# Kernel tuning notes

Measured on AMD Instinct MI355X. Metric: run time of the kernel, lower is better.

## Reference

```python
import jax, jax.numpy as jnp
import numpy as np

NUM_HEADS = 16
R_MIN = 16
R_MAX = 64


def setup_inputs() -> dict:
    key = jax.random.key(0)
    ks = jax.random.split(key, 12)
    bs, S, H = 4, 2048, 1024
    hidden_states = jax.random.normal(ks[0], (bs, S, H), dtype=jnp.float32)
    # Linear layers: y = x @ W.T + b (torch convention, W is [out, in])
    wscale = 1.0 / np.sqrt(H)
    Wq = jax.random.normal(ks[1], (H, H), dtype=jnp.float32) * wscale
    bq = jnp.zeros((H,), dtype=jnp.float32)
    Wk = jax.random.normal(ks[2], (H, H), dtype=jnp.float32) * wscale
    bk = jnp.zeros((H,), dtype=jnp.float32)
    Wv = jax.random.normal(ks[3], (H, H), dtype=jnp.float32) * wscale
    bv = jnp.zeros((H,), dtype=jnp.float32)
    Wo = jax.random.normal(ks[4], (H, H), dtype=jnp.float32) * wscale
    bo = jnp.zeros((H,), dtype=jnp.float32)
    # xavier_uniform for proj_k/proj_v over last two dims (seq_len, r_max)
    xs = float(np.sqrt(6.0 / (S + R_MAX)))
    proj_k = jax.random.uniform(ks[5], (NUM_HEADS, S, R_MAX), dtype=jnp.float32, minval=-xs, maxval=xs)
    proj_v = jax.random.uniform(ks[6], (NUM_HEADS, S, R_MAX), dtype=jnp.float32, minval=-xs, maxval=xs)
    return {
        'hidden_states': hidden_states,
        'Wq': Wq, 'bq': bq, 'Wk': Wk, 'bk': bk, 'Wv': Wv, 'bv': bv,
        'Wo': Wo, 'bo': bo, 'proj_k': proj_k, 'proj_v': proj_v,
    }


def reference(hidden_states, Wq, bq, Wk, bk, Wv, bv, Wo, bo, proj_k, proj_v):
    bs, S, H = hidden_states.shape
    nh = NUM_HEADS
    hd = H // nh

    def heads(x):  # [b,s,H] -> [b,h,s,d]
        return x.reshape(bs, S, nh, hd).transpose(0, 2, 1, 3)

    q = heads(hidden_states @ Wq.T + bq)
    k = heads(hidden_states @ Wk.T + bk)
    v = heads(hidden_states @ Wv.T + bv)

    # dynamic rank from per-sample variance (torch .var is unbiased -> ddof=1)
    batch_var = jnp.var(hidden_states.reshape(bs, -1), axis=1, ddof=1)
    var_norm = (batch_var - batch_var.min()) / (batch_var.max() - batch_var.min() + 1e-6)
    curr_r = jnp.round(R_MIN + var_norm.mean() * (R_MAX - R_MIN)).astype(jnp.int32)

    # low-rank projection of K/V along sequence; compute full r_max, mask at softmax
    key_proj = jnp.einsum('bhld,hlk->bhkd', k, proj_k)      # [b,h,R,d]
    value_proj = jnp.einsum('bhld,hlk->bhkd', v, proj_v)    # [b,h,R,d]

    scores = jnp.einsum('bhsd,bhkd->bhsk', q, key_proj) / jnp.sqrt(jnp.float32(hd))
    rank_mask = jnp.arange(R_MAX) < curr_r                  # [R]
    scores = jnp.where(rank_mask, scores, -jnp.inf)
    attn_probs = jax.nn.softmax(scores, axis=-1)            # zeros beyond curr_r
    # dropout is identity in eval mode
    context = jnp.einsum('bhsk,bhkd->bhsd', attn_probs, value_proj)
    context = context.transpose(0, 2, 1, 3).reshape(bs, S, H)
    output = context @ Wo.T + bo
    return output, attn_probs, curr_r
```

## Files before the change

kernel.cpp:

```cpp
#include <hip/hip_runtime.h>


typedef unsigned short u16;
typedef short s16x8 __attribute__((ext_vector_type(8)));
typedef unsigned short u16x8 __attribute__((ext_vector_type(8)));
typedef unsigned short u16x4 __attribute__((ext_vector_type(4)));
typedef float f32x4 __attribute__((ext_vector_type(4)));

#define GLL16(gp, lp) __builtin_amdgcn_global_load_lds( \
    (const __attribute__((address_space(1))) void*)(gp), \
    (__attribute__((address_space(3))) void*)(lp), 16, 0, 0)

__device__ __forceinline__ u16 f2bf(float f) {
    unsigned u = __float_as_uint(f);
    u += 0x7fffu + ((u >> 16) & 1u);
    return (u16)(u >> 16);
}

__device__ __forceinline__ f32x4 mfma16(s16x8 a, s16x8 b, f32x4 c) {
    return __builtin_amdgcn_mfma_f32_16x16x32_bf16(a, b, c, 0, 0, 0);
}

__global__ __launch_bounds__(256) void prep_k(const float* __restrict__ hs,
        u16* __restrict__ hsb, double* __restrict__ red,
        const float* __restrict__ w0, const float* __restrict__ w1,
        const float* __restrict__ w2, const float* __restrict__ w3,
        u16* __restrict__ wout,
        const float* __restrict__ p0, const float* __restrict__ p1,
        u16* __restrict__ q0, u16* __restrict__ q1,
        const float* __restrict__ bq, const float* __restrict__ bk,
        const float* __restrict__ bv, float* __restrict__ biascat) {
    __shared__ float tl[64][65];
    __shared__ double sa[256], sb[256];
    int bid = blockIdx.x, t = threadIdx.x;
    if (bid < 1024) {
        size_t base = (size_t)bid * 8192;
        double s = 0.0, s2 = 0.0;
        #pragma unroll
        for (int i = 0; i < 4; ++i) {
            size_t idx = base + (size_t)i * 2048 + (size_t)t * 8;
            float4 a = *(const float4*)(hs + idx);
            float4 c = *(const float4*)(hs + idx + 4);
            s  += (double)a.x + (double)a.y + (double)a.z + (double)a.w
                + (double)c.x + (double)c.y + (double)c.z + (double)c.w;
            s2 += (double)a.x * a.x + (double)a.y * a.y + (double)a.z * a.z + (double)a.w * a.w
                + (double)c.x * c.x + (double)c.y * c.y + (double)c.z * c.z + (double)c.w * c.w;
            u16x8 o;
            o[0] = f2bf(a.x); o[1] = f2bf(a.y); o[2] = f2bf(a.z); o[3] = f2bf(a.w);
            o[4] = f2bf(c.x); o[5] = f2bf(c.y); o[6] = f2bf(c.z); o[7] = f2bf(c.w);
            *(u16x8*)(hsb + idx) = o;
        }
        sa[t] = s; sb[t] = s2;
        __syncthreads();
        for (int o = 128; o > 0; o >>= 1) {
            if (t < o) { sa[t] += sa[t + o]; sb[t] += sb[t + o]; }
            __syncthreads();
        }
        if (t == 0) { red[bid * 2] = sa[0]; red[bid * 2 + 1] = sb[0]; }
    } else if (bid < 3072) {
        int bid2 = bid - 1024;
        int mat = bid2 >> 9;
        int off = ((bid2 & 511) * 256 + t) * 8;
        const float* src = (mat == 0) ? w0 : (mat == 1) ? w1 : (mat == 2) ? w2 : w3;
        float4 a = *(const float4*)(src + off);
        float4 c = *(const float4*)(src + off + 4);
        u16x8 o;
        o[0] = f2bf(a.x); o[1] = f2bf(a.y); o[2] = f2bf(a.z); o[3] = f2bf(a.w);
        o[4] = f2bf(c.x); o[5] = f2bf(c.y); o[6] = f2bf(c.z); o[7] = f2bf(c.w);
        *(u16x8*)(wout + (size_t)mat * 1048576 + off) = o;
    } else if (bid < 4096) {
        int bid2 = bid - 3072;
        int which = bid2 >> 9, bi = bid2 & 511;
        const float* p = which ? p1 : p0;
        u16* pt = which ? q1 : q0;
        int h = bi >> 5, lb = bi & 31;
        {
            int l = t >> 2, r0 = (t & 3) * 16;
            const float* src = p + ((size_t)(h * 2048 + lb * 64 + l)) * 64 + r0;
            #pragma unroll
            for (int u = 0; u < 4; ++u) {
                float4 v = *(const float4*)(src + u * 4);
                tl[l][r0 + u * 4 + 0] = v.x; tl[l][r0 + u * 4 + 1] = v.y;
                tl[l][r0 + u * 4 + 2] = v.z; tl[l][r0 + u * 4 + 3] = v.w;
            }
        }
        __syncthreads();
        {
            int r = t >> 2, l0 = (t & 3) * 16;
            u16x8 o0, o1;
            #pragma unroll
            for (int j = 0; j < 8; ++j) { o0[j] = f2bf(tl[l0 + j][r]); o1[j] = f2bf(tl[l0 + 8 + j][r]); }
            u16* dst = pt + ((size_t)(h * 64 + r)) * 2048 + lb * 64 + l0;
            *(u16x8*)dst = o0;
            *(u16x8*)(dst + 8) = o1;
        }
    } else {
        for (int i = t; i < 3072; i += 256) {
            float v = (i < 1024) ? bq[i] : (i < 2048) ? bk[i - 1024] : bv[i - 2048];
            biascat[i] = v;
        }
    }
}

__global__ __launch_bounds__(512, 2) void qkv_gemm_k(const u16* __restrict__ Ag,
        const u16* __restrict__ Wcat, const float* __restrict__ biascat,
        u16* __restrict__ C) {
    __shared__ u16 lds[61440];
    int bid = blockIdx.x;
    int swz = (bid & 7) * 32 + (bid >> 3);
    int bm = swz >> 3, bn = swz & 7;
    int t = threadIdx.x, lane = t & 63, w = t >> 6, wr = w >> 2, wc = w & 3;

    int srow = w * 16 + (lane >> 2);
    int slog = (((lane & 3) ^ ((lane >> 3) & 3)) << 3);
    const u16* asrc0 = Ag + (size_t)(bm * 256 + srow) * 1024 + slog;
    const u16* bsrc0 = Wcat + (size_t)(bn * 384 + srow) * 1024 + slog;

#define STAGEA(kts, h) GLL16(asrc0 + (h) * 131072 + (kts) * 32, \
                             &lds[((kts) % 3) * 20480 + (h) * 4096 + w * 512])
#define STAGEB(kts, h) GLL16(bsrc0 + (h) * 131072 + (kts) * 32, \
                             &lds[((kts) % 3) * 20480 + 8192 + (h) * 4096 + w * 512])

    int pcol = (((lane >> 4) ^ (((lane & 15) >> 1) & 3)) << 3);
    int arow0 = (wr * 128 + (lane & 15)) * 32 + pcol;
    int brow0 = 8192 + (wc * 96 + (lane & 15)) * 32 + pcol;

    f32x4 zero4 = {0.f, 0.f, 0.f, 0.f};
    f32x4 acc[8][6];
    #pragma unroll
    for (int m = 0; m < 8; ++m)
        #pragma unroll
        for (int n = 0; n < 6; ++n) acc[m][n] = zero4;

    STAGEA(0, 0); STAGEA(0, 1); STAGEB(0, 0); STAGEB(0, 1); STAGEB(0, 2);
    STAGEA(1, 0); STAGEA(1, 1); STAGEB(1, 0); STAGEB(1, 1); STAGEB(1, 2);
    asm volatile("s_waitcnt vmcnt(5)" ::: "memory");
    __builtin_amdgcn_s_barrier();
    asm volatile("" ::: "memory");

    for (int kt = 0; kt < 32; ++kt) {
        int b3 = (kt % 3) * 20480;
        int abase = b3 + arow0;
        int bbase = b3 + brow0;
        s16x8 af[8], bf0, bf1, bf2;

        #pragma unroll
        for (int m = 0; m < 8; ++m) af[m] = *(const s16x8*)&lds[abase + m * 512];
        bf0 = *(const s16x8*)&lds[bbase];
        bf1 = *(const s16x8*)&lds[bbase + 512];
        bf2 = *(const s16x8*)&lds[bbase + 1024];
        if (kt < 30) { STAGEA(kt + 2, 0); STAGEA(kt + 2, 1); STAGEB(kt + 2, 0); }
        __builtin_amdgcn_s_barrier();
        asm volatile("s_waitcnt lgkmcnt(0)" ::: "memory");
        __builtin_amdgcn_s_setprio(1);
        #pragma unroll
        for (int m = 0; m < 8; ++m) {
            acc[m][0] = mfma16(af[m], bf0, acc[m][0]);
            acc[m][1] = mfma16(af[m], bf1, acc[m][1]);
            acc[m][2] = mfma16(af[m], bf2, acc[m][2]);
        }
        __builtin_amdgcn_s_setprio(0);
        __builtin_amdgcn_s_barrier();
        asm volatile("" ::: "memory");

        bf0 = *(const s16x8*)&lds[bbase + 1536];
        bf1 = *(const s16x8*)&lds[bbase + 2048];
        bf2 = *(const s16x8*)&lds[bbase + 2560];
        if (kt < 30) { STAGEB(kt + 2, 1); STAGEB(kt + 2, 2); }
        __builtin_amdgcn_s_barrier();
        asm volatile("s_waitcnt lgkmcnt(0)" ::: "memory");
        __builtin_amdgcn_s_setprio(1);
        #pragma unroll
        for (int m = 0; m < 8; ++m) {
            acc[m][3] = mfma16(af[m], bf0, acc[m][3]);
            acc[m][4] = mfma16(af[m], bf1, acc[m][4]);
            acc[m][5] = mfma16(af[m], bf2, acc[m][5]);
        }
        __builtin_amdgcn_s_setprio(0);
        if (kt < 30) { asm volatile("s_waitcnt vmcnt(5)" ::: "memory"); }
        else if (kt == 30) { asm volatile("s_waitcnt vmcnt(0)" ::: "memory"); }
        __builtin_amdgcn_s_barrier();
        asm volatile("" ::: "memory");
    }

    float bias[6];
    #pragma unroll
    for (int n = 0; n < 6; ++n)
        bias[n] = biascat[bn * 384 + wc * 96 + n * 16 + (lane & 15)];
    #pragma unroll
    for (int m = 0; m < 8; ++m) {
        int row0 = bm * 256 + wr * 128 + m * 16 + ((lane >> 4) << 2);
        #pragma unroll
        for (int n = 0; n < 6; ++n) {
            int col = bn * 384 + wc * 96 + n * 16 + (lane & 15);
            #pragma unroll
            for (int v = 0; v < 4; ++v)
                C[(size_t)(row0 + v) * 3072 + col] = f2bf(acc[m][n][v] + bias[n]);
        }
    }
#undef STAGEA
#undef STAGEB
}

__global__ __launch_bounds__(512, 2) void out_gemm_k(const u16* __restrict__ Ag,
        const u16* __restrict__ Bg, const float* __restrict__ biasg,
        float* __restrict__ Cg) {
    __shared__ u16 lds[24576];
    int bid = blockIdx.x;
    int swz = (bid & 7) * 32 + (bid >> 3);
    int bm = swz >> 3, bn = swz & 7;
    int t = threadIdx.x, lane = t & 63, w = t >> 6, wr = w >> 1, wc = w & 1;

    int srow = w * 16 + (lane >> 2);
    int slog = (((lane & 3) ^ ((lane >> 3) & 3)) << 3);
    const u16* asrc0 = Ag + (size_t)(bm * 256 + srow) * 1024 + slog;
    const u16* bsrc0 = Bg + (size_t)(bn * 128 + srow) * 1024 + slog;

#define STAGEA(kts, h) GLL16(asrc0 + (h) * 131072 + (kts) * 32, \
                             &lds[(((kts) & 1) * 8192) + (h) * 4096 + w * 512])
#define STAGEB(kts) GLL16(bsrc0 + (kts) * 32, \
                          &lds[16384 + (((kts) & 1) * 4096) + w * 512])

    int pcol = (((lane >> 4) ^ (((lane & 15) >> 1) & 3)) << 3);
    int arow0 = (wr * 64 + (lane & 15)) * 32 + pcol;
    int brow0 = 16384 + (wc * 64 + (lane & 15)) * 32 + pcol;

    f32x4 zero4 = {0.f, 0.f, 0.f, 0.f};
    f32x4 acc[4][4];
    #pragma unroll
    for (int m = 0; m < 4; ++m)
        #pragma unroll
        for (int n = 0; n < 4; ++n) acc[m][n] = zero4;

    STAGEA(0, 0); STAGEA(0, 1); STAGEB(0);
    STAGEA(1, 0); STAGEA(1, 1);
    asm volatile("s_waitcnt vmcnt(2)" ::: "memory");
    __builtin_amdgcn_s_barrier();
    asm volatile("" ::: "memory");

    for (int kt = 0; kt < 32; ++kt) {
        int abase = (kt & 1) * 8192 + arow0;
        int bbase = (kt & 1) * 4096 + brow0;
        s16x8 af[4], bf0, bf1;

        #pragma unroll
        for (int m = 0; m < 4; ++m) af[m] = *(const s16x8*)&lds[abase + m * 512];
        bf0 = *(const s16x8*)&lds[bbase];
        bf1 = *(const s16x8*)&lds[bbase + 512];
        if (kt < 31) STAGEB(kt + 1);
        asm volatile("s_waitcnt lgkmcnt(0)" ::: "memory");
        __builtin_amdgcn_s_barrier();
        __builtin_amdgcn_s_setprio(1);
        #pragma unroll
        for (int m = 0; m < 4; ++m) {
            acc[m][0] = mfma16(af[m], bf0, acc[m][0]);
            acc[m][1] = mfma16(af[m], bf1, acc[m][1]);
        }
        __builtin_amdgcn_s_setprio(0);
        __builtin_amdgcn_s_barrier();
        asm volatile("" ::: "memory");

        bf0 = *(const s16x8*)&lds[bbase + 1024];
        bf1 = *(const s16x8*)&lds[bbase + 1536];
        if (kt < 30) { STAGEA(kt + 2, 0); STAGEA(kt + 2, 1); }
        if (kt < 30) { asm volatile("s_waitcnt vmcnt(2)" ::: "memory"); }
        else if (kt == 30) { asm volatile("s_waitcnt vmcnt(0)" ::: "memory"); }
        asm volatile("s_waitcnt lgkmcnt(0)" ::: "memory");
        __builtin_amdgcn_s_barrier();
        __builtin_amdgcn_s_setprio(1);
        #pragma unroll
        for (int m = 0; m < 4; ++m) {
            acc[m][2] = mfma16(af[m], bf0, acc[m][2]);
            acc[m][3] = mfma16(af[m], bf1, acc[m][3]);
        }
        __builtin_amdgcn_s_setprio(0);
        __builtin_amdgcn_s_barrier();
        asm volatile("" ::: "memory");
    }

    float bias[4];
    #pragma unroll
    for (int n = 0; n < 4; ++n)
        bias[n] = biasg[bn * 128 + wc * 64 + n * 16 + (lane & 15)];
    #pragma unroll
    for (int m = 0; m < 4; ++m) {
        int row0 = bm * 256 + wr * 64 + m * 16 + ((lane >> 4) << 2);
        #pragma unroll
        for (int n = 0; n < 4; ++n) {
            int col = bn * 128 + wc * 64 + n * 16 + (lane & 15);
            #pragma unroll
            for (int v = 0; v < 4; ++v)
                Cg[(size_t)(row0 + v) * 1024 + col] = acc[m][n][v] + bias[n];
        }
    }
#undef STAGEA
#undef STAGEB
}

__global__ __launch_bounds__(256) void proj_einsum_k(const u16* __restrict__ qkv,
        const u16* __restrict__ pt0, const u16* __restrict__ pt1,
        float* __restrict__ out0, float* __restrict__ out1) {
    __shared__ u16 kt[512 * 66];
    int c = blockIdx.x, h = blockIdx.y, z = blockIdx.z;
    int which = z >> 2, b = z & 3;
    const u16* kv = qkv + 1024 + which * 1024;
    const u16* pt = which ? pt1 : pt0;
    float* outp = which ? out1 : out0;
    int t = threadIdx.x, lane = t & 63, w = t >> 6;

    int tl = t >> 3, sd = (t & 7) * 8;
    const u16* kvp = kv + (size_t)(b * 2048 + c * 512 + tl) * 3072 + h * 64 + sd;
    #pragma unroll
    for (int half = 0; half < 2; ++half) {
        s16x8 g[8];
        #pragma unroll
        for (int i = 0; i < 8; ++i)
            g[i] = *(const s16x8*)(kvp + (size_t)(half * 8 + i) * 98304);
        #pragma unroll
        for (int i = 0; i < 8; ++i)
            *(s16x8*)&kt[(tl + 32 * (half * 8 + i)) * 66 + sd] = g[i];
    }
    __syncthreads();

    f32x4 zero4 = {0.f, 0.f, 0.f, 0.f};
    f32x4 acc[4] = {zero4, zero4, zero4, zero4};
    const u16* ptb_ = pt + (size_t)(h * 64 + (lane & 15)) * 2048 + c * 512 + ((lane >> 4) << 3);
    int gcol = w * 16 + (lane & 15);
    int gk0 = (lane >> 4) << 3;

    #pragma unroll
    for (int ks = 0; ks < 16; ++ks) {
        s16x8 bf;
        int kb = (ks * 32 + gk0) * 66 + gcol;
        #pragma unroll
        for (int j = 0; j < 8; ++j) bf[j] = (short)kt[kb + j * 66];
        #pragma unroll
        for (int m = 0; m < 4; ++m) {
            s16x8 af = *(const s16x8*)(ptb_ + (size_t)m * 32768 + ks * 32);
            acc[m] = mfma16(af, bf, acc[m]);
        }
    }

    float* ob = outp + (size_t)((c * 4 + b) * 16 + h) * 4096;
    #pragma unroll
    for (int m = 0; m < 4; ++m)
        #pragma unroll
        for (int v = 0; v < 4; ++v)
            ob[(m * 16 + ((lane >> 4) << 2) + v) * 64 + w * 16 + (lane & 15)] = acc[m][v];
}

__global__ __launch_bounds__(256) void reduce_kv_k(const float* __restrict__ kp_part,
        const float* __restrict__ vp_part, u16* __restrict__ kpb, u16* __restrict__ vpb,
        const double* __restrict__ red, int* __restrict__ currp, float* __restrict__ outr) {
    int h = blockIdx.x, b = blockIdx.y, zr = blockIdx.z, t = threadIdx.x;
    int r = zr * 16 + (t >> 4), d0 = (t & 15) * 4;
    int base = (b * 16 + h) * 4096 + r * 64 + d0;
    float4 sk = {0.f, 0.f, 0.f, 0.f}, sv = {0.f, 0.f, 0.f, 0.f};
    #pragma unroll
    for (int c = 0; c < 4; ++c) {
        float4 a = *(const float4*)&kp_part[c * 262144 + base];
        float4 g = *(const float4*)&vp_part[c * 262144 + base];
        sk.x += a.x; sk.y += a.y; sk.z += a.z; sk.w += a.w;
        sv.x += g.x; sv.y += g.y; sv.z += g.z; sv.w += g.w;
    }
    size_t ob = (size_t)(b * 16 + h) * 4096;
    u16x4 ok;
    ok[0] = f2bf(sk.x); ok[1] = f2bf(sk.y); ok[2] = f2bf(sk.z); ok[3] = f2bf(sk.w);
    *(u16x4*)&kpb[ob + r * 64 + d0] = ok;
    vpb[ob + (size_t)(d0 + 0) * 64 + r] = f2bf(sv.x);
    vpb[ob + (size_t)(d0 + 1) * 64 + r] = f2bf(sv.y);
    vpb[ob + (size_t)(d0 + 2) * 64 + r] = f2bf(sv.z);
    vpb[ob + (size_t)(d0 + 3) * 64 + r] = f2bf(sv.w);

    if (h == 0 && b == 0 && zr == 0) {
        int lane = t & 63, bb = t >> 6;
        double s = 0.0, s2 = 0.0;
        #pragma unroll
        for (int j = 0; j < 4; ++j) {
            int idx = bb * 256 + j * 64 + lane;
            s += red[idx * 2]; s2 += red[idx * 2 + 1];
        }
        #pragma unroll
        for (int o = 1; o < 64; o <<= 1) { s += __shfl_xor(s, o); s2 += __shfl_xor(s2, o); }
        __shared__ double vs[4];
        if (lane == 0) {
            const double N = 2097152.0;
            vs[bb] = (s2 - s * s / N) / (N - 1.0);
        }
        __syncthreads();
        if (t == 0) {
            double mn = vs[0], mx = vs[0];
            for (int i = 1; i < 4; ++i) { mn = fmin(mn, vs[i]); mx = fmax(mx, vs[i]); }
            double mean = 0.0;
            for (int i = 0; i < 4; ++i) mean += (vs[i] - mn) / (mx - mn + 1e-6);
            mean *= 0.25;
            double rr = rint(16.0 + mean * 48.0);
            *currp = (int)rr;
            *outr = (float)rr;
        }
    }
}

__global__ __launch_bounds__(256) void attn_k(const u16* __restrict__ qkv,
        const u16* __restrict__ kpb, const u16* __restrict__ vpb,
        const int* __restrict__ currp, float* __restrict__ probs, u16* __restrict__ ctxb) {
    int sb = blockIdx.x, h = blockIdx.y, b = blockIdx.z;
    int cr = *currp;
    __shared__ u16 kpl[64 * 80];
    __shared__ u16 vpl[64 * 80];
    __shared__ u16 pl[64 * 80];
    int t = threadIdx.x, lane = t & 63, w = t >> 6;

    {
        int r = t >> 2, d0 = (t & 3) * 16;
        size_t ob = (size_t)(b * 16 + h) * 4096 + t * 16;
        u16x8 k0 = *(const u16x8*)(kpb + ob), k1 = *(const u16x8*)(kpb + ob + 8);
        u16x8 v0 = *(const u16x8*)(vpb + ob), v1 = *(const u16x8*)(vpb + ob + 8);
        *(u16x8*)&kpl[r * 80 + d0]     = k0;
        *(u16x8*)&kpl[r * 80 + d0 + 8] = k1;
        *(u16x8*)&vpl[r * 80 + d0]     = v0;
        *(u16x8*)&vpl[r * 80 + d0 + 8] = v1;
    }
    __syncthreads();

    const u16* qp = qkv + (size_t)(b * 2048 + sb * 64 + w * 16 + (lane & 15)) * 3072 + h * 64 + ((lane >> 4) << 3);
    s16x8 q0 = *(const s16x8*)qp;
    s16x8 q1 = *(const s16x8*)(qp + 32);
    f32x4 zero4 = {0.f, 0.f, 0.f, 0.f};
    f32x4 sc[4];
    #pragma unroll
    for (int j = 0; j < 4; ++j) {
        sc[j] = zero4;
        s16x8 k0 = *(const s16x8*)&kpl[(j * 16 + (lane & 15)) * 80 + ((lane >> 4) << 3)];
        s16x8 k1 = *(const s16x8*)&kpl[(j * 16 + (lane & 15)) * 80 + 32 + ((lane >> 4) << 3)];
        sc[j] = mfma16(q0, k0, sc[j]);
        sc[j] = mfma16(q1, k1, sc[j]);
    }

    const float scale = 0.125f;
    float p_[4][4];
    #pragma unroll
    for (int v = 0; v < 4; ++v) {
        float m = -3.0e38f;
        #pragma unroll
        for (int j = 0; j < 4; ++j) {
            int rr = j * 16 + (lane & 15);
            if (rr < cr) m = fmaxf(m, sc[j][v] * scale);
        }
        m = fmaxf(m, __shfl_xor(m, 1));
        m = fmaxf(m, __shfl_xor(m, 2));
        m = fmaxf(m, __shfl_xor(m, 4));
        m = fmaxf(m, __shfl_xor(m, 8));
        float s = 0.f;
        #pragma unroll
        for (int j = 0; j < 4; ++j) {
            int rr = j * 16 + (lane & 15);
            float p = (rr < cr) ? __expf(sc[j][v] * scale - m) : 0.f;
            p_[j][v] = p; s += p;
        }
        s += __shfl_xor(s, 1); s += __shfl_xor(s, 2);
        s += __shfl_xor(s, 4); s += __shfl_xor(s, 8);
        float inv = 1.f / s;
        #pragma unroll
        for (int j = 0; j < 4; ++j) p_[j][v] *= inv;
    }

    int srow = w * 16 + ((lane >> 4) << 2);
    #pragma unroll
    for (int v = 0; v < 4; ++v) {
        int sg = sb * 64 + srow + v;
        #pragma unroll
        for (int j = 0; j < 4; ++j) {
            int rr = j * 16 + (lane & 15);
            probs[(size_t)((b * 16 + h) * 2048 + sg) * 64 + rr] = p_[j][v];
            pl[(srow + v) * 80 + rr] = f2bf(p_[j][v]);
        }
    }
    __syncthreads();

    f32x4 co[4] = {zero4, zero4, zero4, zero4};
    #pragma unroll
    for (int ks = 0; ks < 2; ++ks) {
        s16x8 pa = *(const s16x8*)&pl[(w * 16 + (lane & 15)) * 80 + ks * 32 + ((lane >> 4) << 3)];
        #pragma unroll
        for (int n = 0; n < 4; ++n) {
            s16x8 vf = *(const s16x8*)&vpl[(n * 16 + (lane & 15)) * 80 + ks * 32 + ((lane >> 4) << 3)];
            co[n] = mfma16(pa, vf, co[n]);
        }
    }
    #pragma unroll
    for (int n = 0; n < 4; ++n)
        #pragma unroll
        for (int v = 0; v < 4; ++v)
            ctxb[(size_t)((b * 2048 + sb * 64 + srow + v) * 16 + h) * 64 + n * 16 + (lane & 15)] = f2bf(co[n][v]);
}

extern "C" void kernel_launch(void* const* d_in, const int* in_sizes, int n_in,
                              void* d_out, int out_size, void* d_ws, size_t ws_size,
                              hipStream_t stream) {
    const float* hs = (const float*)d_in[0];
    const float* Wq = (const float*)d_in[1];
    const float* bq = (const float*)d_in[2];
    const float* Wk = (const float*)d_in[3];
    const float* bk = (const float*)d_in[4];
    const float* Wv = (const float*)d_in[5];
    const float* bv = (const float*)d_in[6];
    const float* Wo = (const float*)d_in[7];
    const float* bo = (const float*)d_in[8];
    const float* pk = (const float*)d_in[9];
    const float* pv = (const float*)d_in[10];
    float* out = (float*)d_out;
    char* w = (char*)d_ws;

    u16* hsb   = (u16*)(w + 0);
    float* vp_part = (float*)(w + 0);
    u16* ctxb  = (u16*)(w + 0);
    u16* wqb   = (u16*)(w + 16777216);
    u16* ptb   = (u16*)(w + 25165824);
    u16* pvtb  = (u16*)(w + 29360128);
    u16* qkvb  = (u16*)(w + 33554432);
    float* kp_part = (float*)(w + 83886080);
    float* biascat = (float*)(w + 92274688);
    double* red    = (double*)(w + 92291072);
    int* currp     = (int*)(w + 92307456);
    u16* kpb   = (u16*)(w + 92307520);
    u16* vpb   = (u16*)(w + 92831808);

    prep_k<<<4097, 256, 0, stream>>>(hs, hsb, red, Wq, Wk, Wv, Wo, wqb,
                                     pk, pv, ptb, pvtb, bq, bk, bv, biascat);

    qkv_gemm_k<<<256, 512, 0, stream>>>(hsb, wqb, biascat, qkvb);

    proj_einsum_k<<<dim3(4, 16, 8), 256, 0, stream>>>(qkvb, ptb, pvtb, kp_part, vp_part);
    reduce_kv_k<<<dim3(16, 4, 4), 256, 0, stream>>>(kp_part, vp_part, kpb, vpb,
                                                    red, currp, out + 16777216);

    attn_k<<<dim3(32, 16, 4), 256, 0, stream>>>(qkvb, kpb, vpb, currp,
                                                out + 8388608, ctxb);

    out_gemm_k<<<256, 512, 0, stream>>>(ctxb, wqb + 3145728, bo, out);
}
```

Baseline: 137.1 us.

## Triple-buffer out GEMM LDS pipeline and stage attention probs for coalesced stores

```diff
diff --git a/kernel.cpp b/kernel.cpp
--- a/kernel.cpp
+++ b/kernel.cpp
@@ -205,7 +205,7 @@
 __global__ __launch_bounds__(512, 2) void out_gemm_k(const u16* __restrict__ Ag,
         const u16* __restrict__ Bg, const float* __restrict__ biasg,
         float* __restrict__ Cg) {
-    __shared__ u16 lds[24576];
+    __shared__ u16 lds[36864];
     int bid = blockIdx.x;
     int swz = (bid & 7) * 32 + (bid >> 3);
     int bm = swz >> 3, bn = swz & 7;
@@ -217,13 +217,13 @@
     const u16* bsrc0 = Bg + (size_t)(bn * 128 + srow) * 1024 + slog;
 
 #define STAGEA(kts, h) GLL16(asrc0 + (h) * 131072 + (kts) * 32, \
-                             &lds[(((kts) & 1) * 8192) + (h) * 4096 + w * 512])
+                             &lds[((kts) % 3) * 12288 + (h) * 4096 + w * 512])
 #define STAGEB(kts) GLL16(bsrc0 + (kts) * 32, \
-                          &lds[16384 + (((kts) & 1) * 4096) + w * 512])
+                          &lds[((kts) % 3) * 12288 + 8192 + w * 512])
 
     int pcol = (((lane >> 4) ^ (((lane & 15) >> 1) & 3)) << 3);
     int arow0 = (wr * 64 + (lane & 15)) * 32 + pcol;
-    int brow0 = 16384 + (wc * 64 + (lane & 15)) * 32 + pcol;
+    int brow0 = 8192 + (wc * 64 + (lane & 15)) * 32 + pcol;
 
     f32x4 zero4 = {0.f, 0.f, 0.f, 0.f};
     f32x4 acc[4][4];
@@ -233,23 +233,24 @@
         for (int n = 0; n < 4; ++n) acc[m][n] = zero4;
 
     STAGEA(0, 0); STAGEA(0, 1); STAGEB(0);
-    STAGEA(1, 0); STAGEA(1, 1);
-    asm volatile("s_waitcnt vmcnt(2)" ::: "memory");
+    STAGEA(1, 0); STAGEA(1, 1); STAGEB(1);
+    asm volatile("s_waitcnt vmcnt(3)" ::: "memory");
     __builtin_amdgcn_s_barrier();
     asm volatile("" ::: "memory");
 
     for (int kt = 0; kt < 32; ++kt) {
-        int abase = (kt & 1) * 8192 + arow0;
-        int bbase = (kt & 1) * 4096 + brow0;
+        int b3 = (kt % 3) * 12288;
+        int abase = b3 + arow0;
+        int bbase = b3 + brow0;
         s16x8 af[4], bf0, bf1;
 
         #pragma unroll
         for (int m = 0; m < 4; ++m) af[m] = *(const s16x8*)&lds[abase + m * 512];
         bf0 = *(const s16x8*)&lds[bbase];
         bf1 = *(const s16x8*)&lds[bbase + 512];
-        if (kt < 31) STAGEB(kt + 1);
+        if (kt < 30) { STAGEA(kt + 2, 0); STAGEA(kt + 2, 1); }
+        __builtin_amdgcn_s_barrier();
         asm volatile("s_waitcnt lgkmcnt(0)" ::: "memory");
-        __builtin_amdgcn_s_barrier();
         __builtin_amdgcn_s_setprio(1);
         #pragma unroll
         for (int m = 0; m < 4; ++m) {
@@ -262,11 +263,9 @@
 
         bf0 = *(const s16x8*)&lds[bbase + 1024];
         bf1 = *(const s16x8*)&lds[bbase + 1536];
-        if (kt < 30) { STAGEA(kt + 2, 0); STAGEA(kt + 2, 1); }
-        if (kt < 30) { asm volatile("s_waitcnt vmcnt(2)" ::: "memory"); }
-        else if (kt == 30) { asm volatile("s_waitcnt vmcnt(0)" ::: "memory"); }
+        if (kt < 30) STAGEB(kt + 2);
+        __builtin_amdgcn_s_barrier();
         asm volatile("s_waitcnt lgkmcnt(0)" ::: "memory");
-        __builtin_amdgcn_s_barrier();
         __builtin_amdgcn_s_setprio(1);
         #pragma unroll
         for (int m = 0; m < 4; ++m) {
@@ -274,6 +273,8 @@
             acc[m][3] = mfma16(af[m], bf1, acc[m][3]);
         }
         __builtin_amdgcn_s_setprio(0);
+        if (kt < 30) { asm volatile("s_waitcnt vmcnt(3)" ::: "memory"); }
+        else if (kt == 30) { asm volatile("s_waitcnt vmcnt(0)" ::: "memory"); }
         __builtin_amdgcn_s_barrier();
         asm volatile("" ::: "memory");
     }
@@ -406,9 +407,9 @@
         const int* __restrict__ currp, float* __restrict__ probs, u16* __restrict__ ctxb) {
     int sb = blockIdx.x, h = blockIdx.y, b = blockIdx.z;
     int cr = *currp;
-    __shared__ u16 kpl[64 * 80];
     __shared__ u16 vpl[64 * 80];
     __shared__ u16 pl[64 * 80];
+    __shared__ __align__(16) u16 kbuf[8192];
     int t = threadIdx.x, lane = t & 63, w = t >> 6;
 
     {
@@ -416,8 +417,8 @@
         size_t ob = (size_t)(b * 16 + h) * 4096 + t * 16;
         u16x8 k0 = *(const u16x8*)(kpb + ob), k1 = *(const u16x8*)(kpb + ob + 8);
         u16x8 v0 = *(const u16x8*)(vpb + ob), v1 = *(const u16x8*)(vpb + ob + 8);
-        *(u16x8*)&kpl[r * 80 + d0]     = k0;
-        *(u16x8*)&kpl[r * 80 + d0 + 8] = k1;
+        *(u16x8*)&kbuf[r * 80 + d0]     = k0;
+        *(u16x8*)&kbuf[r * 80 + d0 + 8] = k1;
         *(u16x8*)&vpl[r * 80 + d0]     = v0;
         *(u16x8*)&vpl[r * 80 + d0 + 8] = v1;
     }
@@ -431,8 +432,8 @@
     #pragma unroll
     for (int j = 0; j < 4; ++j) {
         sc[j] = zero4;
-        s16x8 k0 = *(const s16x8*)&kpl[(j * 16 + (lane & 15)) * 80 + ((lane >> 4) << 3)];
-        s16x8 k1 = *(const s16x8*)&kpl[(j * 16 + (lane & 15)) * 80 + 32 + ((lane >> 4) << 3)];
+        s16x8 k0 = *(const s16x8*)&kbuf[(j * 16 + (lane & 15)) * 80 + ((lane >> 4) << 3)];
+        s16x8 k1 = *(const s16x8*)&kbuf[(j * 16 + (lane & 15)) * 80 + 32 + ((lane >> 4) << 3)];
         sc[j] = mfma16(q0, k0, sc[j]);
         sc[j] = mfma16(q1, k1, sc[j]);
     }
@@ -465,14 +466,16 @@
         for (int j = 0; j < 4; ++j) p_[j][v] *= inv;
     }
 
+    __syncthreads();
+
+    float* pf = (float*)kbuf;
     int srow = w * 16 + ((lane >> 4) << 2);
     #pragma unroll
     for (int v = 0; v < 4; ++v) {
-        int sg = sb * 64 + srow + v;
         #pragma unroll
         for (int j = 0; j < 4; ++j) {
             int rr = j * 16 + (lane & 15);
-            probs[(size_t)((b * 16 + h) * 2048 + sg) * 64 + rr] = p_[j][v];
+            pf[(srow + v) * 64 + rr] = p_[j][v];
             pl[(srow + v) * 80 + rr] = f2bf(p_[j][v]);
         }
     }
@@ -493,6 +496,16 @@
         #pragma unroll
         for (int v = 0; v < 4; ++v)
             ctxb[(size_t)((b * 2048 + sb * 64 + srow + v) * 16 + h) * 64 + n * 16 + (lane & 15)] = f2bf(co[n][v]);
+
+    {
+        int prow = t >> 2, pcol0 = (t & 3) * 16;
+        size_t pbase = (size_t)((b * 16 + h) * 2048 + sb * 64 + prow) * 64 + pcol0;
+        #pragma unroll
+        for (int u = 0; u < 4; ++u) {
+            float4 pv4 = *(const float4*)&pf[prow * 64 + pcol0 + u * 4];
+            *(float4*)&probs[pbase + u * 4] = pv4;
+        }
+    }
 }
 
 extern "C" void kernel_launch(void* const* d_in, const int* in_sizes, int n_in,
```

After: 142.7 us. 1.04x slower.
